# Kernel tuning notes

Hardware: AMD Instinct MI355X
Metric: run time of the kernel (lower is better)

## Reference

```python
import jax, jax.numpy as jnp
import numpy as np

WEIGHT_FACTOR = 0.8


def _pairwise_l2(f):
    # ||a-b|| via GEMM trick: ||a||^2 + ||b||^2 - 2 a.b, avoiding the [N,N,D] blowup.
    sqn = jnp.sum(f * f, axis=1)                      # [N]
    sq = sqn[:, None] + sqn[None, :] - 2.0 * (f @ f.T)  # [N,N]
    sq = jnp.maximum(sq, 0.0)
    pos = sq > 0
    # safe sqrt: subgradient 0 at zero distance (matches torch.norm at 0)
    return jnp.where(pos, jnp.sqrt(jnp.where(pos, sq, 1.0)), 0.0)


def _mse(a, b):
    d = a - b
    return jnp.mean(d * d)


def setup_inputs() -> dict:
    key = jax.random.key(0)
    ks = jax.random.split(key, 8)
    N, D, C = 4096, 256, 1000
    return {
        "pred": jax.random.normal(ks[0], (N, C), dtype=jnp.float32),
        "target": jax.random.normal(ks[1], (N, C), dtype=jnp.float32),
        "pred_f0": jax.random.normal(ks[2], (N, D), dtype=jnp.float32),
        "pred_f1": jax.random.normal(ks[3], (N, D), dtype=jnp.float32),
        "pred_f2": jax.random.normal(ks[4], (N, D), dtype=jnp.float32),
        "target_f0": jax.random.normal(ks[5], (N, D), dtype=jnp.float32),
        "target_f1": jax.random.normal(ks[6], (N, D), dtype=jnp.float32),
        "target_f2": jax.random.normal(ks[7], (N, D), dtype=jnp.float32),
    }


def reference(pred, target, pred_f0, pred_f1, pred_f2, target_f0, target_f1, target_f2):
    pred_feats = (pred_f0, pred_f1, pred_f2)
    target_feats = (target_f0, target_f1, target_f2)
    num_features = len(pred_feats)

    label_loss = _mse(pred, target)
    feature_loss = 0.0
    for pf, tf in zip(pred_feats, target_feats):
        feature_loss = feature_loss + _mse(_pairwise_l2(pf), _pairwise_l2(tf))
    return (1.0 - WEIGHT_FACTOR) * label_loss + WEIGHT_FACTOR * feature_loss / num_features
```

## Files before the change

kernel.cpp:

```cpp
#include <hip/hip_runtime.h>
#include <stdint.h>

#define NR 4096
#define DD 256
#define NC_TOT 4096000
#define TILES 32
#define NTRI 528
#define NBLK_GRAM 512

typedef float f32x4 __attribute__((ext_vector_type(4)));
typedef unsigned char u8;

#define WS_MSEP_OFF  256
#define WS_FEATP_OFF 16384
#define WS_SQN_OFF   32768
#define WS_FP8_OFF   131072

__global__ __launch_bounds__(256) void prep_mse_kernel(
    const float* __restrict__ m0, const float* __restrict__ m1,
    const float* __restrict__ m2, const float* __restrict__ m3,
    const float* __restrict__ m4, const float* __restrict__ m5,
    u8* __restrict__ q8, float* __restrict__ sqn, unsigned* __restrict__ cnt)
{
    const int t = threadIdx.x, w = t >> 6, lane = t & 63;
    const int y = blockIdx.y;
    if (y == 0 && blockIdx.x == 0 && t == 0) *cnt = 0u;

    const float* mp = m0;
    if (y == 1) mp = m1;
    else if (y == 2) mp = m2;
    else if (y == 3) mp = m3;
    else if (y == 4) mp = m4;
    else if (y == 5) mp = m5;
    const int R = blockIdx.x * 4 + w;
    const int P = R >> 7, rr = R & 127;
    const float4* src = (const float4*)(mp + (size_t)R * DD);
    float4 v = src[lane];
    float ss = v.x * v.x + v.y * v.y + v.z * v.z + v.w * v.w;
    unsigned lo = __builtin_amdgcn_cvt_pk_fp8_f32(v.x, v.y, 0u, false);
    unsigned hi = __builtin_amdgcn_cvt_pk_fp8_f32(v.z, v.w, 0u, false);
    unsigned packed = (lo & 0xffffu) | (hi << 16);
    size_t idx = ((size_t)(y * 32 + P) << 15)
                 + (size_t)(lane >> 1) * 1024 + rr * 8 + (lane & 1) * 4;
    *(unsigned*)(q8 + idx) = packed;
    #pragma unroll
    for (int off = 32; off; off >>= 1) ss += __shfl_down(ss, off);
    if (lane == 0) sqn[(size_t)y * NR + R] = ss;
}

#define COMPUTE_STAGE(BI, ACC)                                                 \
  do {                                                                         \
    const u8* tA_ = &buf[BI][0];                                               \
    const u8* tB_ = &buf[BI][16384];                                           \
    __builtin_amdgcn_s_setprio(1);                                             \
    _Pragma("unroll")                                                          \
    for (int kc = 0; kc < 4; kc++) {                                           \
      const int gg = kc * 4 + quad;                                            \
      long a_[4], b_[2];                                                       \
      _Pragma("unroll")                                                        \
      for (int mi = 0; mi < 4; mi++)                                           \
        a_[mi] = *(const long*)&tA_[gg * 1024 + (wm * 64 + mi * 16 + l16) * 8];\
      _Pragma("unroll")                                                        \
      for (int ni = 0; ni < 2; ni++)                                           \
        b_[ni] = *(const long*)&tB_[gg * 1024 + (wn * 32 + ni * 16 + l16) * 8];\
      _Pragma("unroll")                                                        \
      for (int mi = 0; mi < 4; mi++)                                           \
        _Pragma("unroll")                                                      \
        for (int ni = 0; ni < 2; ni++)                                         \
          ACC[mi][ni] = __builtin_amdgcn_mfma_f32_16x16x32_fp8_fp8(            \
              a_[mi], b_[ni], ACC[mi][ni], 0, 0, 0);                           \
    }                                                                          \
    __builtin_amdgcn_s_setprio(0);                                             \
  } while (0)

#define RESET_ACC()                                                            \
  do {                                                                         \
    _Pragma("unroll")                                                          \
    for (int a4 = 0; a4 < 4; a4++)                                             \
      _Pragma("unroll")                                                        \
      for (int b2 = 0; b2 < 2; b2++) {                                         \
        accp[a4][b2] = f32x4{0.f, 0.f, 0.f, 0.f};                              \
        acct[a4][b2] = f32x4{0.f, 0.f, 0.f, 0.f};                              \
      }                                                                        \
  } while (0)

__global__ __launch_bounds__(512, 4) void gram_loss_kernel(
    const u8* __restrict__ q8, const float* __restrict__ sqn,
    const float4* __restrict__ pred, const float4* __restrict__ target,
    float* __restrict__ featp, float* __restrict__ msep,
    unsigned* __restrict__ cnt, float* __restrict__ out)
{
    __shared__ u8 buf[2][32768];
    __shared__ float s_red[8], s_mse[8];
    __shared__ int s_last;

    const int xcd = blockIdx.x & 7, slot = blockIdx.x >> 3;
    const int t = threadIdx.x;
    const int w = t >> 6, lane = t & 63;
    const int wm = w >> 2, wn = w & 3;
    const int quad = lane >> 4, l16 = lane & 15;
    const char* qb = (const char*)q8;

    float mse = 0.f;
    for (int i = blockIdx.x * 512 + t; i < NC_TOT / 4; i += NBLK_GRAM * 512) {
        float4 x = pred[i], yv = target[i];
        float dx = x.x - yv.x, dy = x.y - yv.y;
        float dz = x.z - yv.z, dw = x.w - yv.w;
        mse += dx * dx + dy * dy + dz * dz + dw * dw;
    }

    auto tile_of = [&](int k, int& f, int& ti, int& tj) -> bool {
        int rs = (slot + k * 21 + xcd * 9) & 63;
        int idx = rs + (k << 6), lin;
        if (xcd < 6) {
            if (idx >= 196) return false;
            f = xcd >> 1; lin = (xcd & 1) + 2 * idx;
        } else {
            if (idx >= 204) return false;
            int rr = (xcd - 6) + 2 * idx;
            f = rr / 136; lin = 392 + rr - f * 136;
        }
        int a = 0, rem = lin;
        while (rem >= TILES - a) { rem -= TILES - a; a++; }
        ti = a; tj = a + rem;
        return true;
    };

    auto prefetch = [&](int b, int f, int ti, int tj, int tgt, int kk) {
        const int m = f + 3 * tgt;
        const size_t bA = ((size_t)(m * 32 + ti)) << 15;
        const size_t bB = ((size_t)(m * 32 + tj)) << 15;
        const char* g = qb + ((w < 4) ? bA : bB) + kk * 16384
                        + (w & 3) * 4096 + lane * 16;
        char* l = (char*)&buf[b][0] + ((w < 4) ? 0 : 16384) + (w & 3) * 4096;
        #pragma unroll
        for (int i = 0; i < 4; i++)
            __builtin_amdgcn_global_load_lds(
                (const __attribute__((address_space(1))) void*)(g + i * 1024),
                (__attribute__((address_space(3))) void*)(l + i * 1024), 16, 0, 0);
    };

    f32x4 accp[4][2], acct[4][2];
    RESET_ACC();

    float local = 0.f;

    int fc, tic, tjc;
    tile_of(0, fc, tic, tjc);
    prefetch(0, fc, tic, tjc, 0, 0);
    __syncthreads();

    int k = 0;
    while (true) {
        prefetch(1, fc, tic, tjc, 0, 1);
        COMPUTE_STAGE(0, accp);
        __syncthreads();

        prefetch(0, fc, tic, tjc, 1, 0);
        COMPUTE_STAGE(1, accp);
        __syncthreads();

        prefetch(1, fc, tic, tjc, 1, 1);
        COMPUTE_STAGE(0, acct);
        __syncthreads();

        int fn, tin, tjn;
        const bool more = tile_of(k + 1, fn, tin, tjn);
        if (more) prefetch(0, fn, tin, tjn, 0, 0);
        COMPUTE_STAGE(1, acct);

        {
            const float* sqp = sqn + (size_t)fc * NR;
            const float* sqt = sqn + (size_t)(3 + fc) * NR;
            const bool diag = (tic == tjc);
            float tl = 0.f;
            #pragma unroll
            for (int mi = 0; mi < 4; mi++) {
                const int i0 = wm * 64 + mi * 16 + quad * 4;
                const f32x4 sip = *(const f32x4*)(sqp + tic * 128 + i0);
                const f32x4 sit = *(const f32x4*)(sqt + tic * 128 + i0);
                #pragma unroll
                for (int ni = 0; ni < 2; ni++) {
                    const int j_loc = wn * 32 + ni * 16 + l16;
                    const float spj = sqp[tjc * 128 + j_loc];
                    const float stj = sqt[tjc * 128 + j_loc];
                    const f32x4 gp = accp[mi][ni], gt = acct[mi][ni];
                    #pragma unroll
                    for (int r = 0; r < 4; r++) {
                        float dp2 = fmaxf(fmaf(-2.f, gp[r], sip[r] + spj), 0.f);
                        float dt2 = fmaxf(fmaf(-2.f, gt[r], sit[r] + stj), 0.f);
                        if (diag && (i0 + r == j_loc)) { dp2 = 0.f; dt2 = 0.f; }
                        float sq = __builtin_amdgcn_sqrtf(dp2 * dt2);
                        tl += fmaf(-2.f, sq, dp2 + dt2);
                    }
                }
            }
            local += diag ? tl : 2.f * tl;
            RESET_ACC();
        }
        __syncthreads();
        if (!more) break;
        k++;
        fc = fn; tic = tin; tjc = tjn;
    }

    #pragma unroll
    for (int off = 32; off; off >>= 1) {
        local += __shfl_down(local, off);
        mse   += __shfl_down(mse, off);
    }
    if (lane == 0) { s_red[w] = local; s_mse[w] = mse; }
    __syncthreads();
    if (t == 0) {
        float bs = 0.f, ms = 0.f;
        #pragma unroll
        for (int i = 0; i < 8; i++) { bs += s_red[i]; ms += s_mse[i]; }
        featp[blockIdx.x] = bs;
        msep[blockIdx.x]  = ms;
        __threadfence();
        unsigned old = atomicAdd(cnt, 1u);
        s_last = (old == NBLK_GRAM - 1) ? 1 : 0;
    }
    __syncthreads();

    if (s_last) {
        __threadfence();
        float s2 = 0.f, m2 = 0.f;
        for (int i = t; i < NBLK_GRAM; i += 512) {
            s2 += featp[i];
            m2 += msep[i];
        }
        #pragma unroll
        for (int off = 32; off; off >>= 1) {
            s2 += __shfl_down(s2, off);
            m2 += __shfl_down(m2, off);
        }
        __shared__ float fr[8], mr[8];
        if (lane == 0) { fr[w] = s2; mr[w] = m2; }
        __syncthreads();
        if (t == 0) {
            float fs = 0.f, ms = 0.f;
            #pragma unroll
            for (int i = 0; i < 8; i++) { fs += fr[i]; ms += mr[i]; }
            out[0] = 0.2f * (ms / (float)NC_TOT) +
                     (0.8f / 3.0f) * (fs / ((float)NR * (float)NR));
        }
    }
}

extern "C" void kernel_launch(void* const* d_in, const int* in_sizes, int n_in,
                              void* d_out, int out_size, void* d_ws, size_t ws_size,
                              hipStream_t stream) {
    unsigned* cnt  = (unsigned*)d_ws;
    float* msep    = (float*)((char*)d_ws + WS_MSEP_OFF);
    float* featp   = (float*)((char*)d_ws + WS_FEATP_OFF);
    float* sqn     = (float*)((char*)d_ws + WS_SQN_OFF);
    u8* q8         = (u8*)((char*)d_ws + WS_FP8_OFF);

    prep_mse_kernel<<<dim3(1024, 6), 256, 0, stream>>>(
        (const float*)d_in[2], (const float*)d_in[3], (const float*)d_in[4],
        (const float*)d_in[5], (const float*)d_in[6], (const float*)d_in[7],
        q8, sqn, cnt);

    gram_loss_kernel<<<NBLK_GRAM, 512, 0, stream>>>(
        q8, sqn, (const float4*)d_in[0], (const float4*)d_in[1],
        featp, msep, cnt, (float*)d_out);
}
```

Measured before the change: 139.3 us.

## Fuse fp8 quantization prep into gram kernel behind a grid-wide spin barrier

Moves the per-row fp8 quantization and squared-norm computation from a separate prep kernel into the start of the gram kernel, with each block converting 48 rows. The blocks then meet at a software grid barrier built from an atomic counter, and the label MSE streaming is placed before the wait so it overlaps the barrier. A tiny init kernel now zeroes the counters. This removes a launch and the gap between kernels, but it depends on all 512 blocks being resident at once, otherwise the spin barrier can deadlock.

```diff
diff --git a/kernel.cpp b/kernel.cpp
--- a/kernel.cpp
+++ b/kernel.cpp
@@ -16,36 +16,9 @@
 #define WS_SQN_OFF   32768
 #define WS_FP8_OFF   131072
 
-__global__ __launch_bounds__(256) void prep_mse_kernel(
-    const float* __restrict__ m0, const float* __restrict__ m1,
-    const float* __restrict__ m2, const float* __restrict__ m3,
-    const float* __restrict__ m4, const float* __restrict__ m5,
-    u8* __restrict__ q8, float* __restrict__ sqn, unsigned* __restrict__ cnt)
+__global__ __launch_bounds__(64) void init_kernel(unsigned* __restrict__ cnt)
 {
-    const int t = threadIdx.x, w = t >> 6, lane = t & 63;
-    const int y = blockIdx.y;
-    if (y == 0 && blockIdx.x == 0 && t == 0) *cnt = 0u;
-
-    const float* mp = m0;
-    if (y == 1) mp = m1;
-    else if (y == 2) mp = m2;
-    else if (y == 3) mp = m3;
-    else if (y == 4) mp = m4;
-    else if (y == 5) mp = m5;
-    const int R = blockIdx.x * 4 + w;
-    const int P = R >> 7, rr = R & 127;
-    const float4* src = (const float4*)(mp + (size_t)R * DD);
-    float4 v = src[lane];
-    float ss = v.x * v.x + v.y * v.y + v.z * v.z + v.w * v.w;
-    unsigned lo = __builtin_amdgcn_cvt_pk_fp8_f32(v.x, v.y, 0u, false);
-    unsigned hi = __builtin_amdgcn_cvt_pk_fp8_f32(v.z, v.w, 0u, false);
-    unsigned packed = (lo & 0xffffu) | (hi << 16);
-    size_t idx = ((size_t)(y * 32 + P) << 15)
-                 + (size_t)(lane >> 1) * 1024 + rr * 8 + (lane & 1) * 4;
-    *(unsigned*)(q8 + idx) = packed;
-    #pragma unroll
-    for (int off = 32; off; off >>= 1) ss += __shfl_down(ss, off);
-    if (lane == 0) sqn[(size_t)y * NR + R] = ss;
+    if (threadIdx.x < 16) cnt[threadIdx.x] = 0u;
 }
 
 #define COMPUTE_STAGE(BI, ACC)                                                 \
@@ -85,8 +58,11 @@
   } while (0)
 
 __global__ __launch_bounds__(512, 4) void gram_loss_kernel(
-    const u8* __restrict__ q8, const float* __restrict__ sqn,
+    const float* __restrict__ m0, const float* __restrict__ m1,
+    const float* __restrict__ m2, const float* __restrict__ m3,
+    const float* __restrict__ m4, const float* __restrict__ m5,
     const float4* __restrict__ pred, const float4* __restrict__ target,
+    u8* __restrict__ q8, float* __restrict__ sqn,
     float* __restrict__ featp, float* __restrict__ msep,
     unsigned* __restrict__ cnt, float* __restrict__ out)
 {
@@ -101,6 +77,36 @@
     const int quad = lane >> 4, l16 = lane & 15;
     const char* qb = (const char*)q8;
 
+    {
+        const int base = blockIdx.x * 48;
+        #pragma unroll
+        for (int j = 0; j < 6; j++) {
+            const int flat = base + j * 8 + w;
+            const int mat = flat >> 12, R = flat & 4095;
+            const float* mp = m0;
+            if (mat == 1) mp = m1;
+            else if (mat == 2) mp = m2;
+            else if (mat == 3) mp = m3;
+            else if (mat == 4) mp = m4;
+            else if (mat == 5) mp = m5;
+            const int P = R >> 7, rr = R & 127;
+            float4 v = ((const float4*)(mp + (size_t)R * DD))[lane];
+            float ss = v.x * v.x + v.y * v.y + v.z * v.z + v.w * v.w;
+            unsigned lo = __builtin_amdgcn_cvt_pk_fp8_f32(v.x, v.y, 0u, false);
+            unsigned hi = __builtin_amdgcn_cvt_pk_fp8_f32(v.z, v.w, 0u, false);
+            unsigned packed = (lo & 0xffffu) | (hi << 16);
+            size_t idx = ((size_t)(mat * 32 + P) << 15)
+                         + (size_t)(lane >> 1) * 1024 + rr * 8 + (lane & 1) * 4;
+            *(unsigned*)(q8 + idx) = packed;
+            #pragma unroll
+            for (int off = 32; off; off >>= 1) ss += __shfl_down(ss, off);
+            if (lane == 0) sqn[(size_t)mat * NR + R] = ss;
+        }
+    }
+    __threadfence();
+    __syncthreads();
+    if (t == 0) atomicAdd(&cnt[1], 1u);
+
     float mse = 0.f;
     for (int i = blockIdx.x * 512 + t; i < NC_TOT / 4; i += NBLK_GRAM * 512) {
         float4 x = pred[i], yv = target[i];
@@ -108,6 +114,14 @@
         float dz = x.z - yv.z, dw = x.w - yv.w;
         mse += dx * dx + dy * dy + dz * dz + dw * dw;
     }
+
+    if (t == 0) {
+        while (__hip_atomic_load(&cnt[1], __ATOMIC_ACQUIRE,
+                                 __HIP_MEMORY_SCOPE_AGENT) < (unsigned)NBLK_GRAM)
+            __builtin_amdgcn_s_sleep(2);
+    }
+    __syncthreads();
+    __threadfence();
 
     auto tile_of = [&](int k, int& f, int& ti, int& tj) -> bool {
         int rs = (slot + k * 21 + xcd * 9) & 63;
@@ -132,7 +146,8 @@
         const size_t bB = ((size_t)(m * 32 + tj)) << 15;
         const char* g = qb + ((w < 4) ? bA : bB) + kk * 16384
                         + (w & 3) * 4096 + lane * 16;
-        char* l = (char*)&buf[b][0] + ((w < 4) ? 0 : 16384) + (w & 3) * 4096;
+        char* l = (char*)&buf[0][0] + b * 32768
+                  + ((w < 4) ? 0 : 16384) + (w & 3) * 4096;
         #pragma unroll
         for (int i = 0; i < 4; i++)
             __builtin_amdgcn_global_load_lds(
@@ -218,7 +233,7 @@
         featp[blockIdx.x] = bs;
         msep[blockIdx.x]  = ms;
         __threadfence();
-        unsigned old = atomicAdd(cnt, 1u);
+        unsigned old = atomicAdd(&cnt[0], 1u);
         s_last = (old == NBLK_GRAM - 1) ? 1 : 0;
     }
     __syncthreads();
@@ -257,12 +272,11 @@
     float* sqn     = (float*)((char*)d_ws + WS_SQN_OFF);
     u8* q8         = (u8*)((char*)d_ws + WS_FP8_OFF);
 
-    prep_mse_kernel<<<dim3(1024, 6), 256, 0, stream>>>(
+    init_kernel<<<1, 64, 0, stream>>>(cnt);
+
+    gram_loss_kernel<<<NBLK_GRAM, 512, 0, stream>>>(
         (const float*)d_in[2], (const float*)d_in[3], (const float*)d_in[4],
         (const float*)d_in[5], (const float*)d_in[6], (const float*)d_in[7],
-        q8, sqn, cnt);
-
-    gram_loss_kernel<<<NBLK_GRAM, 512, 0, stream>>>(
-        q8, sqn, (const float4*)d_in[0], (const float4*)d_in[1],
-        featp, msep, cnt, (float*)d_out);
+        (const float4*)d_in[0], (const float4*)d_in[1],
+        q8, sqn, featp, msep, cnt, (float*)d_out);
 }
```

After: 340.1 us. 144% more time.

## Interleave fp8 tile layout for 16-byte LDS reads and zero-init accumulators via MFMA

Applied to the files above, without the earlier changes.

The prep kernel now writes fp8 rows so that pairs of 16-row groups sit side by side. Each lane can then fetch two MFMA operands with one 16-byte LDS load instead of separate 8-byte loads, cutting the number of LDS read instructions in the inner loop by about half. The explicit accumulator reset is removed: the first MFMA of each tile is fed a zero C operand. This saves register moves but ties the prep layout tightly to the compute indexing.

```diff
diff --git a/kernel.cpp b/kernel.cpp
--- a/kernel.cpp
+++ b/kernel.cpp
@@ -9,6 +9,7 @@
 #define NBLK_GRAM 512
 
 typedef float f32x4 __attribute__((ext_vector_type(4)));
+typedef long  v2l  __attribute__((ext_vector_type(2)));
 typedef unsigned char u8;
 
 #define WS_MSEP_OFF  256
@@ -40,15 +41,17 @@
     unsigned lo = __builtin_amdgcn_cvt_pk_fp8_f32(v.x, v.y, 0u, false);
     unsigned hi = __builtin_amdgcn_cvt_pk_fp8_f32(v.z, v.w, 0u, false);
     unsigned packed = (lo & 0xffffu) | (hi << 16);
+    const int rh = rr >> 4;
     size_t idx = ((size_t)(y * 32 + P) << 15)
-                 + (size_t)(lane >> 1) * 1024 + rr * 8 + (lane & 1) * 4;
+                 + (size_t)(lane >> 1) * 1024 + (rh >> 1) * 256
+                 + (rr & 15) * 16 + (rh & 1) * 8 + (lane & 1) * 4;
     *(unsigned*)(q8 + idx) = packed;
     #pragma unroll
     for (int off = 32; off; off >>= 1) ss += __shfl_down(ss, off);
     if (lane == 0) sqn[(size_t)y * NR + R] = ss;
 }
 
-#define COMPUTE_STAGE(BI, ACC)                                                 \
+#define COMPUTE_STAGE(BI, ACC, ZC)                                             \
   do {                                                                         \
     const u8* tA_ = &buf[BI][0];                                               \
     const u8* tB_ = &buf[BI][16384];                                           \
@@ -56,32 +59,24 @@
     _Pragma("unroll")                                                          \
     for (int kc = 0; kc < 4; kc++) {                                           \
       const int gg = kc * 4 + quad;                                            \
-      long a_[4], b_[2];                                                       \
-      _Pragma("unroll")                                                        \
-      for (int mi = 0; mi < 4; mi++)                                           \
-        a_[mi] = *(const long*)&tA_[gg * 1024 + (wm * 64 + mi * 16 + l16) * 8];\
-      _Pragma("unroll")                                                        \
-      for (int ni = 0; ni < 2; ni++)                                           \
-        b_[ni] = *(const long*)&tB_[gg * 1024 + (wn * 32 + ni * 16 + l16) * 8];\
+      v2l av0 = *(const v2l*)&tA_[gg * 1024 + wm * 512 + l16 * 16];            \
+      v2l av1 = *(const v2l*)&tA_[gg * 1024 + wm * 512 + 256 + l16 * 16];      \
+      v2l bv  = *(const v2l*)&tB_[gg * 1024 + wn * 256 + l16 * 16];            \
+      long a_[4] = { av0[0], av0[1], av1[0], av1[1] };                         \
+      long b_[2] = { bv[0], bv[1] };                                           \
       _Pragma("unroll")                                                        \
       for (int mi = 0; mi < 4; mi++)                                           \
         _Pragma("unroll")                                                      \
-        for (int ni = 0; ni < 2; ni++)                                         \
-          ACC[mi][ni] = __builtin_amdgcn_mfma_f32_16x16x32_fp8_fp8(            \
-              a_[mi], b_[ni], ACC[mi][ni], 0, 0, 0);                           \
+        for (int ni = 0; ni < 2; ni++) {                                       \
+          if ((ZC) && kc == 0)                                                 \
+            ACC[mi][ni] = __builtin_amdgcn_mfma_f32_16x16x32_fp8_fp8(          \
+                a_[mi], b_[ni], f32x4{0.f, 0.f, 0.f, 0.f}, 0, 0, 0);           \
+          else                                                                 \
+            ACC[mi][ni] = __builtin_amdgcn_mfma_f32_16x16x32_fp8_fp8(          \
+                a_[mi], b_[ni], ACC[mi][ni], 0, 0, 0);                         \
+        }                                                                      \
     }                                                                          \
     __builtin_amdgcn_s_setprio(0);                                             \
-  } while (0)
-
-#define RESET_ACC()                                                            \
-  do {                                                                         \
-    _Pragma("unroll")                                                          \
-    for (int a4 = 0; a4 < 4; a4++)                                             \
-      _Pragma("unroll")                                                        \
-      for (int b2 = 0; b2 < 2; b2++) {                                         \
-        accp[a4][b2] = f32x4{0.f, 0.f, 0.f, 0.f};                              \
-        acct[a4][b2] = f32x4{0.f, 0.f, 0.f, 0.f};                              \
-      }                                                                        \
   } while (0)
 
 __global__ __launch_bounds__(512, 4) void gram_loss_kernel(
@@ -90,7 +85,7 @@
     float* __restrict__ featp, float* __restrict__ msep,
     unsigned* __restrict__ cnt, float* __restrict__ out)
 {
-    __shared__ u8 buf[2][32768];
+    __shared__ __align__(16) u8 buf[2][32768];
     __shared__ float s_red[8], s_mse[8];
     __shared__ int s_last;
 
@@ -141,8 +136,6 @@
     };
 
     f32x4 accp[4][2], acct[4][2];
-    RESET_ACC();
-
     float local = 0.f;
 
     int fc, tic, tjc;
@@ -153,21 +146,21 @@
     int k = 0;
     while (true) {
         prefetch(1, fc, tic, tjc, 0, 1);
-        COMPUTE_STAGE(0, accp);
+        COMPUTE_STAGE(0, accp, 1);
         __syncthreads();
 
         prefetch(0, fc, tic, tjc, 1, 0);
-        COMPUTE_STAGE(1, accp);
+        COMPUTE_STAGE(1, accp, 0);
         __syncthreads();
 
         prefetch(1, fc, tic, tjc, 1, 1);
-        COMPUTE_STAGE(0, acct);
+        COMPUTE_STAGE(0, acct, 1);
         __syncthreads();
 
         int fn, tin, tjn;
         const bool more = tile_of(k + 1, fn, tin, tjn);
         if (more) prefetch(0, fn, tin, tjn, 0, 0);
-        COMPUTE_STAGE(1, acct);
+        COMPUTE_STAGE(1, acct, 0);
 
         {
             const float* sqp = sqn + (size_t)fc * NR;
@@ -196,7 +189,6 @@
                 }
             }
             local += diag ? tl : 2.f * tl;
-            RESET_ACC();
         }
         __syncthreads();
         if (!more) break;
```

Result: no change. 138.8 us (-0.4%).
